# Kernel optimization log

Measured on AMD Instinct MI355X. Metric: run time of the kernel, lower is better.

The kernel has to match this reference:

```python
import jax, jax.numpy as jnp
import numpy as np

TEMP = 0.025
BN_EPS = 1e-5


def _attention(a, W_in, b_in, g, beta, rm, rv, W_out, b_out):
    # a: (b, n1, n2, P, Q); 1x1 conv over the Q 'channel' dim, gate, softmax over P.
    m = a.mean(axis=3)                                   # (b,n1,n2,Q)
    t = jnp.einsum('bnmq,kq->bnmk', m, W_in) + b_in      # (b,n1,n2,K)
    t = jax.nn.relu((t - rm) / jnp.sqrt(rv + BN_EPS) * g + beta)
    t = jnp.einsum('bnmk,qk->bnmq', t, W_out) + b_out    # (b,n1,n2,Q)
    s = jnp.mean(a * t[:, :, :, None, :], axis=-1)       # (b,n1,n2,P)
    return jax.nn.softmax(s / TEMP, axis=-1) + 1.0


def _cam_forward(zf, xf, conv1_w, conv1_b, bn1_g, bn1_b, bn1_rm, bn1_rv,
                 conv2_w, conv2_b, conv3_w, conv3_b, bn3_g, bn3_b, bn3_rm, bn3_rv,
                 conv4_w, conv4_b):
    out1, out2 = [], []
    L = zf.shape[0]
    for l in range(L):  # small fixed loop over feature levels
        f1, f2 = zf[l], xf[l]
        b, c, h1, w1 = f1.shape
        h2, w2 = f2.shape[2], f2.shape[3]
        P, Q = h1 * w1, h2 * w2
        f1s = jnp.stack([f1.reshape(b, c, P)] * 2, axis=1)   # (b,2,c,P)
        f2s = jnp.stack([f2.reshape(b, c, Q)] * 2, axis=1)   # (b,2,c,Q)
        f1n = f1s / jnp.maximum(jnp.linalg.norm(f1s, axis=2, keepdims=True), 1e-12)
        f2n = f2s / jnp.maximum(jnp.linalg.norm(f2s, axis=2, keepdims=True), 1e-12)
        a1 = jnp.einsum('bncp,bmcq->bnmpq', f1n, f2n)        # (b,2,2,P,Q)
        att1 = _attention(a1, conv1_w, conv1_b, bn1_g, bn1_b, bn1_rm, bn1_rv,
                          conv2_w, conv2_b)                  # (b,2,2,P)
        att2 = _attention(a1.swapaxes(3, 4), conv3_w, conv3_b, bn3_g, bn3_b,
                          bn3_rm, bn3_rv, conv4_w, conv4_b)  # (b,2,2,Q)
        # mean over the (n1,n2)=(2,2) pair grid without materializing (b,2,2,c,HW)
        o1 = jnp.einsum('bncp,bnmp->bcp', f1s, att1) / 4.0
        o2 = jnp.einsum('bmcq,bnmq->bcq', f2s, att2) / 4.0
        out1.append(o1.reshape(b, c, h1, w1))
        out2.append(o2.reshape(b, c, h2, w2))
    return (jnp.stack(out1), jnp.stack(out2))


def setup_inputs() -> dict:
    key = jax.random.key(0)
    ks = jax.random.split(key, 12)
    L, B, C = 3, 32, 256
    inp = {
        'zf': jax.random.normal(ks[0], (L, B, C, 7, 7), jnp.float32),
        'xf': jax.random.normal(ks[1], (L, B, C, 31, 31), jnp.float32),
        'conv1_w': jax.random.normal(ks[2], (31, 961), jnp.float32) * np.sqrt(2.0 / 31),
        'conv1_b': jax.random.normal(ks[3], (31,), jnp.float32) * 0.05,
        'bn1_g': jax.random.uniform(ks[4], (31,), jnp.float32, 0.5, 1.5),
        'bn1_b': jax.random.normal(ks[5], (31,), jnp.float32) * 0.05,
        'bn1_rm': jnp.zeros((31,), jnp.float32),
        'bn1_rv': jnp.ones((31,), jnp.float32),
        'conv2_w': jax.random.normal(ks[6], (961, 31), jnp.float32) * np.sqrt(2.0 / 961),
        'conv2_b': jax.random.normal(ks[7], (961,), jnp.float32) * 0.05,
        'conv3_w': jax.random.normal(ks[8], (7, 49), jnp.float32) * np.sqrt(2.0 / 7),
        'conv3_b': jax.random.normal(ks[9], (7,), jnp.float32) * 0.05,
        'bn3_g': jax.random.uniform(ks[10], (7,), jnp.float32, 0.5, 1.5),
        'bn3_b': jax.random.normal(ks[11], (7,), jnp.float32) * 0.05,
        'bn3_rm': jnp.zeros((7,), jnp.float32),
        'bn3_rv': jnp.ones((7,), jnp.float32),
        'conv4_w': jax.random.normal(jax.random.fold_in(key, 100), (49, 7), jnp.float32) * np.sqrt(2.0 / 49),
        'conv4_b': jax.random.normal(jax.random.fold_in(key, 101), (49,), jnp.float32) * 0.05,
    }
    return inp


def reference(zf, xf, conv1_w, conv1_b, bn1_g, bn1_b, bn1_rm, bn1_rv,
              conv2_w, conv2_b, conv3_w, conv3_b, bn3_g, bn3_b, bn3_rm, bn3_rv,
              conv4_w, conv4_b):
    return _cam_forward(zf, xf, conv1_w, conv1_b, bn1_g, bn1_b, bn1_rm, bn1_rv,
                        conv2_w, conv2_b, conv3_w, conv3_b, bn3_g, bn3_b,
                        bn3_rm, bn3_rv, conv4_w, conv4_b)
```

## Files before the change

kernel.cpp:

```cpp
#include <hip/hip_runtime.h>
#include <math.h>

#define NLB 96
#define CC  256
#define PP  49
#define QQ  961
#define TEMP_INV 40.0f
#define BN_EPS 1e-5f

#define N1 (NLB*CC*PP)
#define N2 (NLB*CC*QQ)

typedef __attribute__((ext_vector_type(8))) short bf16x8;
typedef __attribute__((ext_vector_type(4))) float f32x4;
typedef __attribute__((ext_vector_type(8))) unsigned short ushort8;

__device__ inline unsigned short f2bf(float x) {
    unsigned int u = __float_as_uint(x);
    unsigned int r = (u + 0x7fffu + ((u >> 16) & 1u)) >> 16;
    return (unsigned short)r;
}

__device__ __forceinline__ void gload_lds4(const float* g, float* l) {
    __builtin_amdgcn_global_load_lds(
        (const __attribute__((address_space(1))) void*)g,
        (__attribute__((address_space(3))) void*)l,
        4, 0, 0);
}

__global__ __launch_bounds__(256) void prep_z(
    const float* __restrict__ zf, unsigned short* __restrict__ f1T,
    float* __restrict__ inv1_ws, float* __restrict__ mrow_ws)
{
    const int lb = blockIdx.x;
    if (threadIdx.x < PP) mrow_ws[lb * PP + threadIdx.x] = 0.f;

    const float* __restrict__ f1 = zf + (size_t)lb * CC * PP;
    const int p  = threadIdx.x >> 2;
    const int qu = threadIdx.x & 3;
    const int c0 = qu * 64;
    float ss = 0.f;
    ushort8* dst = (ushort8*)(f1T + ((size_t)lb * 64 + p) * CC + c0);
#pragma unroll
    for (int s = 0; s < 8; ++s) {
        unsigned short tmp[8];
#pragma unroll
        for (int j = 0; j < 8; ++j) {
            const float v = (p < PP) ? f1[(size_t)(c0 + s * 8 + j) * PP + p] : 0.f;
            ss = fmaf(v, v, ss);
            tmp[j] = f2bf(v);
        }
        dst[s] = *(ushort8*)tmp;
    }
    ss += __shfl_xor(ss, 1, 64);
    ss += __shfl_xor(ss, 2, 64);
    if (qu == 0) inv1_ws[lb * 64 + p] = (p < PP) ? 1.0f / fmaxf(sqrtf(ss), 1e-12f) : 0.f;
}

#define STAGE(BUF, KC)                                                         \
    {                                                                          \
        const int c0s = (KC) * 64 + wave * 8;                                  \
        _Pragma("unroll")                                                      \
        for (int r8 = 0; r8 < 8; ++r8) {                                       \
            _Pragma("unroll")                                                  \
            for (int h = 0; h < 2; ++h) {                                      \
                const int qi = ng * 128 + h * 64 + lane;                       \
                const int qc2 = qi < QQ ? qi : QQ - 1;                         \
                gload_lds4(f2 + (size_t)(c0s + r8) * QQ + qc2,                 \
                           &BUF[(wave * 8 + r8) * 128 + h * 64]);              \
            }                                                                  \
        }                                                                      \
    }

#define COMPS(BUF, KC)                                                         \
    {                                                                          \
        bf16x8 af[4][2];                                                       \
        _Pragma("unroll")                                                      \
        for (int mt = 0; mt < 4; ++mt)                                         \
            _Pragma("unroll")                                                  \
            for (int ks = 0; ks < 2; ++ks)                                     \
                af[mt][ks] = *(const bf16x8*)&f1L[(mt * 16 + l15) * 264 +      \
                                                  (KC) * 64 + ks * 32 + g4 * 8];\
        _Pragma("unroll")                                                      \
        for (int ks = 0; ks < 2; ++ks) {                                       \
            unsigned short us[8];                                              \
            _Pragma("unroll")                                                  \
            for (int j = 0; j < 8; ++j) {                                      \
                const float v = BUF[(ks * 32 + g4 * 8 + j) * 128 + wq + l15];  \
                ss2 = fmaf(v, v, ss2);                                         \
                us[j] = f2bf(v);                                               \
            }                                                                  \
            const bf16x8 bfr = *(const bf16x8*)us;                             \
            _Pragma("unroll")                                                  \
            for (int mt = 0; mt < 4; ++mt)                                     \
                acc[mt] = __builtin_amdgcn_mfma_f32_16x16x32_bf16(             \
                    af[mt][ks], bfr, acc[mt], 0, 0, 0);                        \
        }                                                                      \
    }

__global__ __launch_bounds__(512) void corr_mfma(
    const unsigned short* __restrict__ f1T, const float* __restrict__ xf,
    const float* __restrict__ inv1_ws,
    float* __restrict__ A_all, float* __restrict__ mcol_ws,
    float* __restrict__ mrow_ws)
{
    const int ng = blockIdx.x;
    const int lb = blockIdx.y;
    const int tid  = threadIdx.x;
    const int lane = tid & 63;
    const int wave = tid >> 6;
    const int g4   = lane >> 4;
    const int l15  = lane & 15;
    const int wq   = wave * 16;

    const float* __restrict__ f2 = xf + (size_t)lb * CC * QQ;

    __shared__ __align__(16) unsigned short f1L[64 * 264];
    __shared__ float inv1L[64];
    __shared__ __align__(16) float bufA[64 * 128];
    __shared__ __align__(16) float bufB[64 * 128];

    STAGE(bufA, 0)
    for (int i = tid; i < 64 * 32; i += 512) {
        const int row = i >> 5, seg = i & 31;
        *(ushort8*)&f1L[row * 264 + seg * 8] =
            *(const ushort8*)&f1T[((size_t)lb * 64 + row) * CC + seg * 8];
    }
    if (tid < 64) inv1L[tid] = inv1_ws[lb * 64 + tid];
    __syncthreads();

    const int qg = ng * 128 + wq + l15;
    const bool qv = (qg < QQ);

    f32x4 acc[4];
#pragma unroll
    for (int mt = 0; mt < 4; ++mt) acc[mt] = (f32x4)0.f;
    float ss2 = 0.f;

    STAGE(bufB, 1)
    COMPS(bufA, 0)
    __syncthreads();
    STAGE(bufA, 2)
    COMPS(bufB, 1)
    __syncthreads();
    STAGE(bufB, 3)
    COMPS(bufA, 2)
    __syncthreads();
    COMPS(bufB, 3)

    float ssf = ss2;
    ssf += __shfl_xor(ssf, 16, 64);
    ssf += __shfl_xor(ssf, 32, 64);
    const float iv2 = 1.0f / fmaxf(sqrtf(ssf), 1e-12f);

    float* __restrict__ Aout = A_all + (size_t)lb * PP * QQ;
    float vv[16];
    float cs = 0.f;
#pragma unroll
    for (int mt = 0; mt < 4; ++mt)
#pragma unroll
        for (int r = 0; r < 4; ++r) {
            const int p = mt * 16 + g4 * 4 + r;
            const float v = qv ? acc[mt][r] * inv1L[p] * iv2 : 0.f;
            vv[mt * 4 + r] = v;
            cs += v;
            if (p < PP && qv) Aout[(size_t)p * QQ + qg] = v;
        }
    cs += __shfl_xor(cs, 16, 64);
    cs += __shfl_xor(cs, 32, 64);
    if ((lane < 16) && qv) mcol_ws[lb * QQ + qg] = cs;
#pragma unroll
    for (int mt = 0; mt < 4; ++mt)
#pragma unroll
        for (int r = 0; r < 4; ++r) {
            const int p = mt * 16 + g4 * 4 + r;
            float s = vv[mt * 4 + r];
            s += __shfl_xor(s, 1, 64);
            s += __shfl_xor(s, 2, 64);
            s += __shfl_xor(s, 4, 64);
            s += __shfl_xor(s, 8, 64);
            if (((lane & 15) == 0) && p < PP) atomicAdd(&mrow_ws[lb * PP + p], s);
        }
}

__global__ __launch_bounds__(512) void attn_kernel(
    const float* __restrict__ A_all,
    const float* __restrict__ mcol_ws, const float* __restrict__ mrow_ws,
    const float* __restrict__ W1, const float* __restrict__ b1,
    const float* __restrict__ g1, const float* __restrict__ bb1,
    const float* __restrict__ rm1, const float* __restrict__ rv1,
    const float* __restrict__ W2, const float* __restrict__ b2,
    const float* __restrict__ W3, const float* __restrict__ b3,
    const float* __restrict__ g3, const float* __restrict__ bb3,
    const float* __restrict__ rm3, const float* __restrict__ rv3,
    const float* __restrict__ W4, const float* __restrict__ b4,
    float* __restrict__ att1_ws, float* __restrict__ att2_ws)
{
    const int lb = blockIdx.x;
    const float* __restrict__ A = A_all + (size_t)lb * PP * QQ;
    const int tid  = threadIdx.x;
    const int lane = tid & 63;
    const int wv   = tid >> 6;

    __shared__ float mcolL[QQ];
    __shared__ float mrowL[PP];
    __shared__ float taL[31], tbL[7];
    __shared__ float t2aL[QQ], t2bL[PP];
    __shared__ float s2sL[QQ];
    __shared__ float s1L[PP];
    __shared__ float redM[8], redS[8];

    for (int q = tid; q < QQ; q += 512) mcolL[q] = mcol_ws[lb * QQ + q] * (1.0f / PP);
    if (tid < PP) mrowL[tid] = mrow_ws[lb * PP + tid] * (1.0f / QQ);
    __syncthreads();

    if (tid < 31 * 16) {
        const int k = tid >> 4, sub = tid & 15;
        float s = 0.f;
        for (int q = sub; q < QQ; q += 16) s = fmaf(mcolL[q], W1[k * QQ + q], s);
        s += __shfl_xor(s, 1, 64); s += __shfl_xor(s, 2, 64);
        s += __shfl_xor(s, 4, 64); s += __shfl_xor(s, 8, 64);
        if (sub == 0) {
            float t = s + b1[k];
            t = (t - rm1[k]) * rsqrtf(rv1[k] + BN_EPS) * g1[k] + bb1[k];
            taL[k] = fmaxf(t, 0.f);
        }
    }
    if (tid < 7 * 8) {
        const int k = tid >> 3, sub = tid & 7;
        float s = 0.f;
        for (int p = sub; p < PP; p += 8) s = fmaf(mrowL[p], W3[k * PP + p], s);
        s += __shfl_xor(s, 1, 64); s += __shfl_xor(s, 2, 64); s += __shfl_xor(s, 4, 64);
        if (sub == 0) {
            float t = s + b3[k];
            t = (t - rm3[k]) * rsqrtf(rv3[k] + BN_EPS) * g3[k] + bb3[k];
            tbL[k] = fmaxf(t, 0.f);
        }
    }
    __syncthreads();

    for (int q = tid; q < QQ; q += 512) {
        float s = b2[q];
#pragma unroll
        for (int k = 0; k < 31; ++k) s = fmaf(taL[k], W2[q * 31 + k], s);
        t2aL[q] = s;
    }
    if (tid < PP) {
        float s = b4[tid];
#pragma unroll
        for (int k = 0; k < 7; ++k) s = fmaf(tbL[k], W4[tid * 7 + k], s);
        t2bL[tid] = s;
    }
    __syncthreads();

    for (int q = tid; q < QQ; q += 512) {
        float s = 0.f;
#pragma unroll
        for (int p = 0; p < PP; ++p) s = fmaf(A[(size_t)p * QQ + q], t2bL[p], s);
        s2sL[q] = s * (1.0f / PP) * TEMP_INV;
    }
    for (int p = wv; p < PP; p += 8) {
        float s = 0.f;
        for (int q = lane; q < QQ; q += 64) s = fmaf(A[(size_t)p * QQ + q], t2aL[q], s);
        for (int off = 32; off > 0; off >>= 1) s += __shfl_xor(s, off, 64);
        if (lane == 0) s1L[p] = s * (1.0f / QQ) * TEMP_INV;
    }
    __syncthreads();

    if (wv == 0) {
        const float v = (lane < PP) ? s1L[lane] : -3.4e38f;
        float m = v;
        for (int off = 32; off > 0; off >>= 1) m = fmaxf(m, __shfl_xor(m, off, 64));
        const float e = (lane < PP) ? expf(v - m) : 0.f;
        float sum = e;
        for (int off = 32; off > 0; off >>= 1) sum += __shfl_xor(sum, off, 64);
        if (lane < PP) att1_ws[lb * PP + lane] = e / sum + 1.0f;
    }

    float lm = -3.4e38f;
    for (int q = tid; q < QQ; q += 512) lm = fmaxf(lm, s2sL[q]);
    for (int off = 32; off > 0; off >>= 1) lm = fmaxf(lm, __shfl_xor(lm, off, 64));
    if (lane == 0) redM[wv] = lm;
    __syncthreads();
    float gm = redM[0];
#pragma unroll
    for (int i = 1; i < 8; ++i) gm = fmaxf(gm, redM[i]);
    float ls = 0.f;
    for (int q = tid; q < QQ; q += 512) ls += expf(s2sL[q] - gm);
    for (int off = 32; off > 0; off >>= 1) ls += __shfl_xor(ls, off, 64);
    if (lane == 0) redS[wv] = ls;
    __syncthreads();
    float tot = 0.f;
#pragma unroll
    for (int i = 0; i < 8; ++i) tot += redS[i];
    const float rinv = 1.0f / tot;
    for (int q = tid; q < QQ; q += 512)
        att2_ws[lb * QQ + q] = expf(s2sL[q] - gm) * rinv + 1.0f;
}

template <int INNER>
__global__ __launch_bounds__(256) void scale_kernel(
    const float* __restrict__ in, const float* __restrict__ att,
    float* __restrict__ out, int n4)
{
    const int i = blockIdx.x * 256 + threadIdx.x;
    if (i >= n4) return;
    const float4 v = reinterpret_cast<const float4*>(in)[i];
    const float* vv = reinterpret_cast<const float*>(&v);
    float4 o;
    float* ov = reinterpret_cast<float*>(&o);
    const int g = i * 4;
#pragma unroll
    for (int j = 0; j < 4; ++j) {
        const int gg = g + j;
        const int lb = gg / (CC * INNER);
        const int x  = gg % INNER;
        ov[j] = vv[j] * att[lb * INNER + x];
    }
    reinterpret_cast<float4*>(out)[i] = o;
}

extern "C" void kernel_launch(void* const* d_in, const int* in_sizes, int n_in,
                              void* d_out, int out_size, void* d_ws, size_t ws_size,
                              hipStream_t stream)
{
    const float* zf  = (const float*)d_in[0];
    const float* xf  = (const float*)d_in[1];
    const float* W1  = (const float*)d_in[2];
    const float* b1  = (const float*)d_in[3];
    const float* g1  = (const float*)d_in[4];
    const float* bb1 = (const float*)d_in[5];
    const float* rm1 = (const float*)d_in[6];
    const float* rv1 = (const float*)d_in[7];
    const float* W2  = (const float*)d_in[8];
    const float* b2  = (const float*)d_in[9];
    const float* W3  = (const float*)d_in[10];
    const float* b3  = (const float*)d_in[11];
    const float* g3  = (const float*)d_in[12];
    const float* bb3 = (const float*)d_in[13];
    const float* rm3 = (const float*)d_in[14];
    const float* rv3 = (const float*)d_in[15];
    const float* W4  = (const float*)d_in[16];
    const float* b4  = (const float*)d_in[17];

    char* wsb = (char*)d_ws;
    unsigned short* f1T = (unsigned short*)wsb;
    float* fbase = (float*)(f1T + (size_t)NLB * 64 * CC);
    float* A     = fbase;
    float* att1  = A + (size_t)NLB * PP * QQ;
    float* att2  = att1 + (size_t)NLB * PP;
    float* mcol  = att2 + (size_t)NLB * QQ;
    float* mrow  = mcol + (size_t)NLB * QQ;
    float* inv1  = mrow + (size_t)NLB * PP;

    float* out1 = (float*)d_out;
    float* out2 = out1 + N1;

    prep_z<<<NLB, 256, 0, stream>>>(zf, f1T, inv1, mrow);

    dim3 gcorr(8, NLB);
    corr_mfma<<<gcorr, 512, 0, stream>>>(f1T, xf, inv1, A, mcol, mrow);

    attn_kernel<<<NLB, 512, 0, stream>>>(A, mcol, mrow,
        W1, b1, g1, bb1, rm1, rv1, W2, b2,
        W3, b3, g3, bb3, rm3, rv3, W4, b4,
        att1, att2);

    const int n4_1 = N1 / 4;
    const int n4_2 = N2 / 4;
    scale_kernel<PP><<<(n4_1 + 255) / 256, 256, 0, stream>>>(zf, att1, out1, n4_1);
    scale_kernel<QQ><<<(n4_2 + 255) / 256, 256, 0, stream>>>(xf, att2, out2, n4_2);
}
```

Measured before the change: 146.7 us.

## Widen corr tile to 256 columns, single-buffer K-chunks, aggregate row sums in LDS

The correlation kernel now gives each block 256 q-columns (two 16-column tiles per wave) instead of 128, which halves the grid and reuses each A-fragment load for twice as many MFMAs. The double-buffered 64-channel stages become a single padded 32-channel buffer walked over 8 serialized stage/compute steps, so global loads no longer overlap with compute. Row sums are first reduced in shared memory and then written with one global atomic per row, cutting global atomic traffic. The cost is fewer blocks (384) on a large GPU, more synchronisation points and the loss of load/compute overlap.

```diff
diff --git a/kernel.cpp b/kernel.cpp
--- a/kernel.cpp
+++ b/kernel.cpp
@@ -57,44 +57,43 @@
     if (qu == 0) inv1_ws[lb * 64 + p] = (p < PP) ? 1.0f / fmaxf(sqrtf(ss), 1e-12f) : 0.f;
 }
 
-#define STAGE(BUF, KC)                                                         \
+#define STAGE(K)                                                               \
     {                                                                          \
-        const int c0s = (KC) * 64 + wave * 8;                                  \
+        const int c0s = (K) * 32 + wave * 4;                                   \
         _Pragma("unroll")                                                      \
-        for (int r8 = 0; r8 < 8; ++r8) {                                       \
+        for (int r = 0; r < 4; ++r) {                                          \
             _Pragma("unroll")                                                  \
-            for (int h = 0; h < 2; ++h) {                                      \
-                const int qi = ng * 128 + h * 64 + lane;                       \
-                const int qc2 = qi < QQ ? qi : QQ - 1;                         \
-                gload_lds4(f2 + (size_t)(c0s + r8) * QQ + qc2,                 \
-                           &BUF[(wave * 8 + r8) * 128 + h * 64]);              \
+            for (int i = 0; i < 4; ++i) {                                      \
+                const int qcol = q0 + i * 64 + lane;                           \
+                const int qc2 = qcol < QQ ? qcol : QQ - 1;                     \
+                gload_lds4(f2 + (size_t)(c0s + r) * QQ + qc2,                  \
+                           &buf[(wave * 4 + r) * 260 + i * 64]);               \
             }                                                                  \
         }                                                                      \
     }
 
-#define COMPS(BUF, KC)                                                         \
+#define COMPS(K)                                                               \
     {                                                                          \
-        bf16x8 af[4][2];                                                       \
+        bf16x8 af[4];                                                          \
         _Pragma("unroll")                                                      \
         for (int mt = 0; mt < 4; ++mt)                                         \
-            _Pragma("unroll")                                                  \
-            for (int ks = 0; ks < 2; ++ks)                                     \
-                af[mt][ks] = *(const bf16x8*)&f1L[(mt * 16 + l15) * 264 +      \
-                                                  (KC) * 64 + ks * 32 + g4 * 8];\
+            af[mt] = *(const bf16x8*)&f1L[(mt * 16 + l15) * 264 +              \
+                                          (K) * 32 + g4 * 8];                  \
         _Pragma("unroll")                                                      \
-        for (int ks = 0; ks < 2; ++ks) {                                       \
+        for (int i = 0; i < 2; ++i) {                                          \
+            const int qloc = (wave + 8 * i) * 16 + l15;                        \
             unsigned short us[8];                                              \
             _Pragma("unroll")                                                  \
             for (int j = 0; j < 8; ++j) {                                      \
-                const float v = BUF[(ks * 32 + g4 * 8 + j) * 128 + wq + l15];  \
-                ss2 = fmaf(v, v, ss2);                                         \
+                const float v = buf[(g4 * 8 + j) * 260 + qloc];                \
+                ss2[i] = fmaf(v, v, ss2[i]);                                   \
                 us[j] = f2bf(v);                                               \
             }                                                                  \
             const bf16x8 bfr = *(const bf16x8*)us;                             \
             _Pragma("unroll")                                                  \
             for (int mt = 0; mt < 4; ++mt)                                     \
-                acc[mt] = __builtin_amdgcn_mfma_f32_16x16x32_bf16(             \
-                    af[mt][ks], bfr, acc[mt], 0, 0, 0);                        \
+                acc[i][mt] = __builtin_amdgcn_mfma_f32_16x16x32_bf16(          \
+                    af[mt], bfr, acc[i][mt], 0, 0, 0);                         \
         }                                                                      \
     }
 
@@ -111,76 +110,81 @@
     const int wave = tid >> 6;
     const int g4   = lane >> 4;
     const int l15  = lane & 15;
-    const int wq   = wave * 16;
+    const int q0   = ng * 256;
 
     const float* __restrict__ f2 = xf + (size_t)lb * CC * QQ;
 
     __shared__ __align__(16) unsigned short f1L[64 * 264];
     __shared__ float inv1L[64];
-    __shared__ __align__(16) float bufA[64 * 128];
-    __shared__ __align__(16) float bufB[64 * 128];
-
-    STAGE(bufA, 0)
+    __shared__ float mrowL[64];
+    __shared__ __align__(16) float buf[32 * 260];
+
+    if (tid < 64) { inv1L[tid] = inv1_ws[lb * 64 + tid]; mrowL[tid] = 0.f; }
+    STAGE(0)
     for (int i = tid; i < 64 * 32; i += 512) {
         const int row = i >> 5, seg = i & 31;
         *(ushort8*)&f1L[row * 264 + seg * 8] =
             *(const ushort8*)&f1T[((size_t)lb * 64 + row) * CC + seg * 8];
     }
-    if (tid < 64) inv1L[tid] = inv1_ws[lb * 64 + tid];
-    __syncthreads();
-
-    const int qg = ng * 128 + wq + l15;
-    const bool qv = (qg < QQ);
-
-    f32x4 acc[4];
-#pragma unroll
-    for (int mt = 0; mt < 4; ++mt) acc[mt] = (f32x4)0.f;
-    float ss2 = 0.f;
-
-    STAGE(bufB, 1)
-    COMPS(bufA, 0)
-    __syncthreads();
-    STAGE(bufA, 2)
-    COMPS(bufB, 1)
-    __syncthreads();
-    STAGE(bufB, 3)
-    COMPS(bufA, 2)
-    __syncthreads();
-    COMPS(bufB, 3)
-
-    float ssf = ss2;
-    ssf += __shfl_xor(ssf, 16, 64);
-    ssf += __shfl_xor(ssf, 32, 64);
-    const float iv2 = 1.0f / fmaxf(sqrtf(ssf), 1e-12f);
+    __syncthreads();
+
+    f32x4 acc[2][4];
+#pragma unroll
+    for (int i = 0; i < 2; ++i)
+#pragma unroll
+        for (int mt = 0; mt < 4; ++mt) acc[i][mt] = (f32x4)0.f;
+    float ss2[2] = {0.f, 0.f};
+
+#pragma unroll
+    for (int k = 0; k < 8; ++k) {
+        COMPS(k)
+        __syncthreads();
+        if (k < 7) {
+            STAGE(k + 1)
+            __syncthreads();
+        }
+    }
 
     float* __restrict__ Aout = A_all + (size_t)lb * PP * QQ;
-    float vv[16];
-    float cs = 0.f;
-#pragma unroll
-    for (int mt = 0; mt < 4; ++mt)
-#pragma unroll
-        for (int r = 0; r < 4; ++r) {
-            const int p = mt * 16 + g4 * 4 + r;
-            const float v = qv ? acc[mt][r] * inv1L[p] * iv2 : 0.f;
-            vv[mt * 4 + r] = v;
-            cs += v;
-            if (p < PP && qv) Aout[(size_t)p * QQ + qg] = v;
-        }
-    cs += __shfl_xor(cs, 16, 64);
-    cs += __shfl_xor(cs, 32, 64);
-    if ((lane < 16) && qv) mcol_ws[lb * QQ + qg] = cs;
-#pragma unroll
-    for (int mt = 0; mt < 4; ++mt)
-#pragma unroll
-        for (int r = 0; r < 4; ++r) {
-            const int p = mt * 16 + g4 * 4 + r;
-            float s = vv[mt * 4 + r];
-            s += __shfl_xor(s, 1, 64);
-            s += __shfl_xor(s, 2, 64);
-            s += __shfl_xor(s, 4, 64);
-            s += __shfl_xor(s, 8, 64);
-            if (((lane & 15) == 0) && p < PP) atomicAdd(&mrow_ws[lb * PP + p], s);
-        }
+#pragma unroll
+    for (int i = 0; i < 2; ++i) {
+        const int qg = q0 + (wave + 8 * i) * 16 + l15;
+        const bool qv = (qg < QQ);
+        float ssf = ss2[i];
+        ssf += __shfl_xor(ssf, 16, 64);
+        ssf += __shfl_xor(ssf, 32, 64);
+        const float iv2 = 1.0f / fmaxf(sqrtf(ssf), 1e-12f);
+
+        float vv[16];
+        float cs = 0.f;
+#pragma unroll
+        for (int mt = 0; mt < 4; ++mt)
+#pragma unroll
+            for (int r = 0; r < 4; ++r) {
+                const int p = mt * 16 + g4 * 4 + r;
+                const float v = qv ? acc[i][mt][r] * inv1L[p] * iv2 : 0.f;
+                vv[mt * 4 + r] = v;
+                cs += v;
+                if (p < PP && qv) Aout[(size_t)p * QQ + qg] = v;
+            }
+        cs += __shfl_xor(cs, 16, 64);
+        cs += __shfl_xor(cs, 32, 64);
+        if ((lane < 16) && qv) mcol_ws[lb * QQ + qg] = cs;
+#pragma unroll
+        for (int mt = 0; mt < 4; ++mt)
+#pragma unroll
+            for (int r = 0; r < 4; ++r) {
+                const int p = mt * 16 + g4 * 4 + r;
+                float s = vv[mt * 4 + r];
+                s += __shfl_xor(s, 1, 64);
+                s += __shfl_xor(s, 2, 64);
+                s += __shfl_xor(s, 4, 64);
+                s += __shfl_xor(s, 8, 64);
+                if (((lane & 15) == 0) && p < PP) atomicAdd(&mrowL[p], s);
+            }
+    }
+    __syncthreads();
+    if (tid < PP) atomicAdd(&mrow_ws[lb * PP + tid], mrowL[tid]);
 }
 
 __global__ __launch_bounds__(512) void attn_kernel(
@@ -358,7 +362,7 @@
 
     prep_z<<<NLB, 256, 0, stream>>>(zf, f1T, inv1, mrow);
 
-    dim3 gcorr(8, NLB);
+    dim3 gcorr(4, NLB);
     corr_mfma<<<gcorr, 512, 0, stream>>>(f1T, xf, inv1, A, mcol, mrow);
 
     attn_kernel<<<NLB, 512, 0, stream>>>(A, mcol, mrow,
```

New measurement: 127.5 us. 1.15x faster.
